# Kernel optimization log

Measured on AMD Instinct MI355X. Metric: run time of the kernel, lower is better.

The kernel has to match this reference:

```python
import jax, jax.numpy as jnp
import numpy as np

B, S, D, H, E = 4, 2048, 512, 1024, 8


def setup_inputs() -> dict:
    key = jax.random.key(0)
    ks = jax.random.split(key, 4)
    x = jax.random.normal(ks[0], (B, S, D), jnp.float32)
    Wr = jax.random.normal(ks[1], (E, D), jnp.float32) * 0.02   # router weight [E, D]
    br = jnp.zeros((E,), jnp.float32)
    W1 = jax.random.normal(ks[2], (E, D, H), jnp.float32) * 0.02  # fc1 per expert
    b1 = jnp.zeros((E, H), jnp.float32)
    W2 = jax.random.normal(ks[3], (E, H, D), jnp.float32) * 0.02  # fc2 per expert
    b2 = jnp.zeros((E, D), jnp.float32)
    return {"x": x, "Wr": Wr, "br": br, "W1": W1, "b1": b1, "W2": W2, "b2": b2}


def reference(x, Wr, br, W1, b1, W2, b2):
    # world_size == 1: every all_to_all is the identity; the pipeline reduces to
    # y[t] = sum_{k in top2} gate_k(t) * Expert_{idx_k(t)}(x[t])
    b, s, d = x.shape
    n = b * s
    e = Wr.shape[0]
    xf = x.reshape(n, d)                                   # (N, D)
    logits = xf @ Wr.T + br                                # (N, E)
    probs = jax.nn.softmax(logits, axis=-1)
    top2_prob, top2_idx = jax.lax.top_k(probs, 2)          # (N, 2) each, same tie-break as torch.topk
    # combine weights: comb[t, e] = sum_k gate_tk * [idx_tk == e]
    comb = jnp.zeros((n, e), x.dtype).at[jnp.arange(n)[:, None], top2_idx].add(top2_prob)
    # dense grouped-expert FFN (exact erf-GELU, matching torch F.gelu default)
    h = jax.nn.gelu(jnp.einsum('nd,edh->enh', xf, W1) + b1[:, None, :], approximate=False)
    o = jnp.einsum('enh,ehd->end', h, W2) + b2[:, None, :]  # (E, N, D)
    y = jnp.einsum('ne,end->nd', comb, o)                   # gate-weighted combine
    return y.reshape(b, s, d)
```

## Files before the change

### kernel.cpp

```cpp
#include <hip/hip_runtime.h>
#include <hip/hip_bf16.h>
#include <math.h>

#define N_TOK 8192
#define DIM   512
#define HID   1024
#define NEXP  8
#define CSTRIDE 32
#define NBLK  32
#define TCAP  80

typedef __attribute__((ext_vector_type(8))) __bf16 bf16x8;
typedef __attribute__((ext_vector_type(4))) float  f32x4;

static __device__ __forceinline__ unsigned short f2bf(float f) {
    unsigned int u = __builtin_bit_cast(unsigned int, f);
    unsigned int r = u + 0x7fffu + ((u >> 16) & 1u);
    return (unsigned short)(r >> 16);
}
static __device__ __forceinline__ float bf2f(unsigned short s) {
    unsigned int u = ((unsigned int)s) << 16;
    return __builtin_bit_cast(float, u);
}

__global__ __launch_bounds__(256) void prep_router_kernel(
    const float* __restrict__ x, const float* __restrict__ Wr,
    const float* __restrict__ br,
    const float* __restrict__ W1, const float* __restrict__ W2,
    unsigned short* __restrict__ xb,
    unsigned short* __restrict__ W1p, unsigned short* __restrict__ W2p,
    int* __restrict__ counts, int* __restrict__ tlist, float* __restrict__ glist)
{
    __shared__ unsigned short lt[32][128];
    __shared__ float lg[32][8];
    __shared__ int lcnt[8];
    __shared__ int lbase[8];
    int bid = blockIdx.x;
    int tin = threadIdx.x;
    if (bid < 2048) {
        int e, kb, seg, OUTD;
        const float* W;
        if (bid < 1024) {
            e = bid >> 7; kb = (bid >> 3) & 15; seg = bid & 7;
            OUTD = HID;
            W = W1 + (size_t)e * DIM * HID + (size_t)(kb * 32) * HID + seg * 128;
        } else {
            int b = bid - 1024;
            e = b >> 7; kb = (b >> 2) & 31; seg = b & 3;
            OUTD = DIM;
            W = W2 + (size_t)e * HID * DIM + (size_t)(kb * 32) * DIM + seg * 128;
        }
        #pragma unroll
        for (int i = 0; i < 4; i++) {
            int fl = i * 256 + tin;
            int r = fl >> 5, c4 = fl & 31;
            float4 v = *reinterpret_cast<const float4*>(W + (size_t)r * OUTD + c4 * 4);
            lt[r][c4*4+0] = f2bf(v.x); lt[r][c4*4+1] = f2bf(v.y);
            lt[r][c4*4+2] = f2bf(v.z); lt[r][c4*4+3] = f2bf(v.w);
        }
        __syncthreads();
        unsigned short* dstp = (bid < 1024) ? W1p : W2p;
        #pragma unroll
        for (int i = 0; i < 2; i++) {
            int s = i * 256 + tin;
            int nbl = s >> 6, l = s & 63;
            unsigned short u[8];
            #pragma unroll
            for (int j = 0; j < 8; j++) u[j] = lt[(l >> 4) * 8 + j][nbl * 16 + (l & 15)];
            size_t o;
            if (bid < 1024) o = (((size_t)((bid>>7) * 64 + (bid&7) * 8 + nbl) * 16 + ((bid>>3)&15)) * 64 + l) * 8;
            else { int b2_ = bid - 1024;
                   o = (((size_t)((b2_>>7) * 32 + (b2_&3) * 8 + nbl) * 32 + ((b2_>>2)&31)) * 64 + l) * 8; }
            *reinterpret_cast<uint4*>(dstp + o) = *reinterpret_cast<const uint4*>(u);
        }
        return;
    }
    int rb = bid - 2048;
    int slot = tin >> 3, e = tin & 7;
    int t0 = rb * 32;
    int t = t0 + slot;
    if (tin < 8) lcnt[tin] = 0;
    const float4* xr = (const float4*)(x + (size_t)t * DIM);
    const float4* wr = (const float4*)(Wr + (size_t)e * DIM);
    float acc = 0.f;
    #pragma unroll 4
    for (int i = 0; i < DIM / 4; i++) {
        float4 a = xr[i], b = wr[i];
        acc += a.x * b.x + a.y * b.y + a.z * b.z + a.w * b.w;
    }
    acc += br[e];
    lg[slot][e] = acc;
    __syncthreads();
    int i1 = 0, i2 = 0, l1 = 0, l2 = 0;
    float p1 = 0.f, p2 = 0.f;
    if (e == 0) {
        float l0[8];
        #pragma unroll
        for (int i = 0; i < 8; i++) l0[i] = lg[slot][i];
        float m1 = l0[0];
        #pragma unroll
        for (int i = 1; i < 8; i++) if (l0[i] > m1) { m1 = l0[i]; i1 = i; }
        float sum = 0.f;
        #pragma unroll
        for (int i = 0; i < 8; i++) sum += expf(l0[i] - m1);
        float m2 = -1e30f;
        #pragma unroll
        for (int i = 0; i < 8; i++) if (i != i1 && l0[i] > m2) { m2 = l0[i]; i2 = i; }
        float inv = 1.f / sum;
        p1 = inv;
        p2 = expf(m2 - m1) * inv;
        l1 = atomicAdd(&lcnt[i1], 1);
        l2 = atomicAdd(&lcnt[i2], 1);
    }
    __syncthreads();
    if (tin < 8) lbase[tin] = atomicAdd(&counts[tin * CSTRIDE], lcnt[tin]);
    __syncthreads();
    if (e == 0) {
        int pos1 = lbase[i1] + l1;
        tlist[i1 * N_TOK + pos1] = t * 2;     glist[i1 * N_TOK + pos1] = p1;
        int pos2 = lbase[i2] + l2;
        tlist[i2 * N_TOK + pos2] = t * 2 + 1; glist[i2 * N_TOK + pos2] = p2;
    }
    #pragma unroll
    for (int i = 0; i < 8; i++) {
        int flat = i * 256 + tin;
        int row = flat >> 6, c8 = flat & 63;
        const float4* src = (const float4*)(x + (size_t)(t0 + row) * DIM + c8 * 8);
        float4 a = src[0], b = src[1];
        unsigned short u[8];
        u[0]=f2bf(a.x); u[1]=f2bf(a.y); u[2]=f2bf(a.z); u[3]=f2bf(a.w);
        u[4]=f2bf(b.x); u[5]=f2bf(b.y); u[6]=f2bf(b.z); u[7]=f2bf(b.w);
        *reinterpret_cast<uint4*>(xb + (size_t)(t0 + row) * DIM + c8 * 8) =
            *reinterpret_cast<const uint4*>(u);
    }
}

__global__ __launch_bounds__(512, 2) void ffn_kernel(
    const unsigned short* __restrict__ xb,
    const unsigned short* __restrict__ W1p,
    const unsigned short* __restrict__ W2p,
    const float* __restrict__ b1, const float* __restrict__ b2,
    const int* __restrict__ counts, const int* __restrict__ tlist,
    const float* __restrict__ glist, unsigned short* __restrict__ opair)
{
    const int e = blockIdx.x;
    const int cnt = counts[e * CSTRIDE];
    const int ty = blockIdx.y;
    const int m0 = (cnt * ty) >> 5;
    const int m1 = (cnt * (ty + 1)) >> 5;
    const int nvalid = m1 - m0;
    if (nvalid <= 0) return;

    __shared__ __align__(16) unsigned short xs[TCAP * 512];
    __shared__ __align__(16) unsigned short hs[TCAP * 256];
    __shared__ int   tls[TCAP];
    __shared__ float gls[TCAP];

    const int tid = threadIdx.x;
    const int w = tid >> 6, lane = tid & 63;
    const int lg_ = lane >> 4, lm = lane & 15;

    if (tid < TCAP) {
        int idx = m0 + tid;
        int src = (idx < m1) ? idx : m0;
        tls[tid] = tlist[e * N_TOK + src];
        gls[tid] = (idx < m1) ? glist[e * N_TOK + src] : 0.f;
    }
    __syncthreads();

    #pragma unroll
    for (int i = 0; i < 10; i++) {
        int row = w * 10 + i;
        uint4 v;
        if (row < nvalid) {
            int token = tls[row] >> 1;
            v = *(reinterpret_cast<const uint4*>(xb + (size_t)token * DIM) + lane);
        } else {
            v.x = v.y = v.z = v.w = 0u;
        }
        int bo = row * 1024 + ((lane * 16) ^ ((row & 7) << 4));
        *reinterpret_cast<uint4*>(reinterpret_cast<char*>(xs) + bo) = v;
    }
    __syncthreads();

    const char* xsb = reinterpret_cast<const char*>(xs);
    char* hsb = reinterpret_cast<char*>(hs);

    f32x4 acc2[4][5];
    #pragma unroll
    for (int a = 0; a < 4; a++)
        #pragma unroll
        for (int b = 0; b < 5; b++) acc2[a][b] = (f32x4)0.f;

    for (int c = 0; c < 4; c++) {
        f32x4 acc1[2][5];
        #pragma unroll
        for (int a = 0; a < 2; a++)
            #pragma unroll
            for (int b = 0; b < 5; b++) acc1[a][b] = (f32x4)0.f;
        const uint4* w1base = reinterpret_cast<const uint4*>(W1p)
            + ((size_t)(e * 64 + c * 16 + w * 2) * 16) * 64 + lane;
        #pragma unroll
        for (int kb = 0; kb < 16; kb++) {
            bf16x8 aw[2];
            #pragma unroll
            for (int i = 0; i < 2; i++)
                aw[i] = __builtin_bit_cast(bf16x8, w1base[(size_t)(i * 16 + kb) * 64]);
            #pragma unroll
            for (int tt = 0; tt < 5; tt++) {
                int row = tt * 16 + lm;
                int bo = row * 1024 + ((kb * 64 + lg_ * 16) ^ ((row & 7) << 4));
                bf16x8 bx = __builtin_bit_cast(bf16x8,
                    *reinterpret_cast<const uint4*>(xsb + bo));
                #pragma unroll
                for (int i = 0; i < 2; i++)
                    acc1[i][tt] = __builtin_amdgcn_mfma_f32_16x16x32_bf16(aw[i], bx, acc1[i][tt], 0, 0, 0);
            }
        }
        __syncthreads();
        #pragma unroll
        for (int i = 0; i < 2; i++) {
            int hloc0 = (w * 2 + i) * 16 + lg_ * 4;
            f32x4 b1v = *reinterpret_cast<const f32x4*>(b1 + (size_t)e * HID + c * 256 + hloc0);
            #pragma unroll
            for (int tt = 0; tt < 5; tt++) {
                int trow = tt * 16 + lm;
                float g[4];
                #pragma unroll
                for (int r = 0; r < 4; r++) {
                    float v = acc1[i][tt][r] + b1v[r];
                    g[r] = 0.5f * v * (1.f + erff(v * 0.7071067811865475f));
                }
                unsigned int p0 = (unsigned int)f2bf(g[0]) | ((unsigned int)f2bf(g[1]) << 16);
                unsigned int p1 = (unsigned int)f2bf(g[2]) | ((unsigned int)f2bf(g[3]) << 16);
                unsigned long long pk = (unsigned long long)p0 | ((unsigned long long)p1 << 32);
                int bo = trow * 512 + ((hloc0 * 2) ^ ((trow & 7) << 4));
                *reinterpret_cast<unsigned long long*>(hsb + bo) = pk;
            }
        }
        __syncthreads();
        const uint4* w2base = reinterpret_cast<const uint4*>(W2p)
            + ((size_t)(e * 32 + w * 4) * 32 + c * 8) * 64 + lane;
        #pragma unroll
        for (int kb = 0; kb < 8; kb++) {
            bf16x8 aw2[4];
            #pragma unroll
            for (int j = 0; j < 4; j++)
                aw2[j] = __builtin_bit_cast(bf16x8, w2base[(size_t)(j * 32 + kb) * 64]);
            #pragma unroll
            for (int tt = 0; tt < 5; tt++) {
                int row = tt * 16 + lm;
                int bo = row * 512 + ((kb * 64 + lg_ * 16) ^ ((row & 7) << 4));
                bf16x8 bh = __builtin_bit_cast(bf16x8,
                    *reinterpret_cast<const uint4*>(hsb + bo));
                #pragma unroll
                for (int j = 0; j < 4; j++)
                    acc2[j][tt] = __builtin_amdgcn_mfma_f32_16x16x32_bf16(aw2[j], bh, acc2[j][tt], 0, 0, 0);
            }
        }
    }

    #pragma unroll
    for (int j = 0; j < 4; j++) {
        int dbase = (w * 4 + j) * 16 + lg_ * 4;
        f32x4 b2v = *reinterpret_cast<const f32x4*>(b2 + (size_t)e * DIM + dbase);
        #pragma unroll
        for (int tt = 0; tt < 5; tt++) {
            int trow = tt * 16 + lm;
            if (trow < nvalid) {
                int   ent = tls[trow];
                float gt  = gls[trow];
                float o0 = gt * (acc2[j][tt][0] + b2v[0]);
                float o1 = gt * (acc2[j][tt][1] + b2v[1]);
                float o2 = gt * (acc2[j][tt][2] + b2v[2]);
                float o3 = gt * (acc2[j][tt][3] + b2v[3]);
                uint2 pk;
                pk.x = (unsigned int)f2bf(o0) | ((unsigned int)f2bf(o1) << 16);
                pk.y = (unsigned int)f2bf(o2) | ((unsigned int)f2bf(o3) << 16);
                *reinterpret_cast<uint2*>(opair + (size_t)ent * DIM + dbase) = pk;
            }
        }
    }
}

__global__ __launch_bounds__(256) void combine_kernel(
    const unsigned short* __restrict__ opair, float* __restrict__ y)
{
    int n = blockIdx.x * 256 + threadIdx.x;
    int t = n >> 6, c8 = n & 63;
    uint4 a = *reinterpret_cast<const uint4*>(opair + (size_t)(t * 2) * DIM + c8 * 8);
    uint4 b = *reinterpret_cast<const uint4*>(opair + (size_t)(t * 2 + 1) * DIM + c8 * 8);
    float4 r0, r1;
    r0.x = bf2f((unsigned short)(a.x      )) + bf2f((unsigned short)(b.x      ));
    r0.y = bf2f((unsigned short)(a.x >> 16)) + bf2f((unsigned short)(b.x >> 16));
    r0.z = bf2f((unsigned short)(a.y      )) + bf2f((unsigned short)(b.y      ));
    r0.w = bf2f((unsigned short)(a.y >> 16)) + bf2f((unsigned short)(b.y >> 16));
    r1.x = bf2f((unsigned short)(a.z      )) + bf2f((unsigned short)(b.z      ));
    r1.y = bf2f((unsigned short)(a.z >> 16)) + bf2f((unsigned short)(b.z >> 16));
    r1.z = bf2f((unsigned short)(a.w      )) + bf2f((unsigned short)(b.w      ));
    r1.w = bf2f((unsigned short)(a.w >> 16)) + bf2f((unsigned short)(b.w >> 16));
    float4* dst = reinterpret_cast<float4*>(y + (size_t)t * DIM + c8 * 8);
    dst[0] = r0; dst[1] = r1;
}

extern "C" void kernel_launch(void* const* d_in, const int* in_sizes, int n_in,
                              void* d_out, int out_size, void* d_ws, size_t ws_size,
                              hipStream_t stream)
{
    const float* x  = (const float*)d_in[0];
    const float* Wr = (const float*)d_in[1];
    const float* br = (const float*)d_in[2];
    const float* W1 = (const float*)d_in[3];
    const float* b1 = (const float*)d_in[4];
    const float* W2 = (const float*)d_in[5];
    const float* b2 = (const float*)d_in[6];
    float* y = (float*)d_out;

    char* ws = (char*)d_ws;
    int*   counts = (int*)ws;
    int*   tlist  = (int*)(ws + 1024);
    float* glist  = (float*)(ws + 1024 + 262144);
    unsigned short* xb  = (unsigned short*)(ws + 1024 + 524288);
    unsigned short* W1p = xb  + (size_t)N_TOK * DIM;
    unsigned short* W2p = W1p + (size_t)NEXP * DIM * HID;
    unsigned short* opair = W2p + (size_t)NEXP * HID * DIM;

    hipMemsetAsync(counts, 0, NEXP * CSTRIDE * sizeof(int), stream);
    prep_router_kernel<<<2304, 256, 0, stream>>>(x, Wr, br, W1, W2, xb,
                                                 W1p, W2p, counts, tlist, glist);
    ffn_kernel<<<dim3(8, NBLK), 512, 0, stream>>>(xb, W1p, W2p, b1, b2,
                                                  counts, tlist, glist, opair);
    combine_kernel<<<2048, 256, 0, stream>>>(opair, y);
}
```

Measured before the change: 122.0 us.

## Fuse x bf16 conversion into FFN gather and restructure router block layout

Drops the separate bf16 copy of x. The FFN kernel now gathers fp32 token rows and converts them to bf16 while loading into shared memory. The router now runs first, on 256 blocks, with 8 lanes per token splitting the D dimension and reducing by shuffle, and weight-packing blocks are reordered so the expert index varies fastest. The FFN also skips MFMA work for 16-row tiles beyond the valid token count and drops the 2-block occupancy hint. This saves a write and re-read of x in bf16, but the FFN gather now reads twice the bytes per token.

```diff
diff --git a/kernel.cpp b/kernel.cpp
--- a/kernel.cpp
+++ b/kernel.cpp
@@ -27,116 +27,113 @@
     const float* __restrict__ x, const float* __restrict__ Wr,
     const float* __restrict__ br,
     const float* __restrict__ W1, const float* __restrict__ W2,
-    unsigned short* __restrict__ xb,
     unsigned short* __restrict__ W1p, unsigned short* __restrict__ W2p,
     int* __restrict__ counts, int* __restrict__ tlist, float* __restrict__ glist)
 {
     __shared__ unsigned short lt[32][128];
-    __shared__ float lg[32][8];
     __shared__ int lcnt[8];
     __shared__ int lbase[8];
     int bid = blockIdx.x;
     int tin = threadIdx.x;
-    if (bid < 2048) {
-        int e, kb, seg, OUTD;
-        const float* W;
-        if (bid < 1024) {
-            e = bid >> 7; kb = (bid >> 3) & 15; seg = bid & 7;
-            OUTD = HID;
-            W = W1 + (size_t)e * DIM * HID + (size_t)(kb * 32) * HID + seg * 128;
-        } else {
-            int b = bid - 1024;
-            e = b >> 7; kb = (b >> 2) & 31; seg = b & 3;
-            OUTD = DIM;
-            W = W2 + (size_t)e * HID * DIM + (size_t)(kb * 32) * DIM + seg * 128;
-        }
-        #pragma unroll
-        for (int i = 0; i < 4; i++) {
-            int fl = i * 256 + tin;
-            int r = fl >> 5, c4 = fl & 31;
-            float4 v = *reinterpret_cast<const float4*>(W + (size_t)r * OUTD + c4 * 4);
-            lt[r][c4*4+0] = f2bf(v.x); lt[r][c4*4+1] = f2bf(v.y);
-            lt[r][c4*4+2] = f2bf(v.z); lt[r][c4*4+3] = f2bf(v.w);
-        }
-        __syncthreads();
-        unsigned short* dstp = (bid < 1024) ? W1p : W2p;
-        #pragma unroll
-        for (int i = 0; i < 2; i++) {
-            int s = i * 256 + tin;
-            int nbl = s >> 6, l = s & 63;
-            unsigned short u[8];
-            #pragma unroll
-            for (int j = 0; j < 8; j++) u[j] = lt[(l >> 4) * 8 + j][nbl * 16 + (l & 15)];
-            size_t o;
-            if (bid < 1024) o = (((size_t)((bid>>7) * 64 + (bid&7) * 8 + nbl) * 16 + ((bid>>3)&15)) * 64 + l) * 8;
-            else { int b2_ = bid - 1024;
-                   o = (((size_t)((b2_>>7) * 32 + (b2_&3) * 8 + nbl) * 32 + ((b2_>>2)&31)) * 64 + l) * 8; }
-            *reinterpret_cast<uint4*>(dstp + o) = *reinterpret_cast<const uint4*>(u);
+    if (bid < 256) {
+        int slot = tin >> 3, es = tin & 7;
+        int t = bid * 32 + slot;
+        if (tin < 8) lcnt[tin] = 0;
+        const float4* xr = (const float4*)(x + (size_t)t * DIM + es * 64);
+        float4 xv[16];
+        #pragma unroll
+        for (int i = 0; i < 16; i++) xv[i] = xr[i];
+        float part[8];
+        #pragma unroll
+        for (int ed = 0; ed < 8; ed++) {
+            const float4* wrp = (const float4*)(Wr + (size_t)ed * DIM + es * 64);
+            float a = 0.f;
+            #pragma unroll
+            for (int i = 0; i < 16; i++) {
+                float4 b = wrp[i];
+                a += xv[i].x*b.x + xv[i].y*b.y + xv[i].z*b.z + xv[i].w*b.w;
+            }
+            part[ed] = a;
+        }
+        #pragma unroll
+        for (int m = 1; m < 8; m <<= 1) {
+            #pragma unroll
+            for (int ed = 0; ed < 8; ed++)
+                part[ed] += __shfl_xor(part[ed], m, 64);
+        }
+        int i1 = 0, i2 = 0, l1 = 0, l2 = 0;
+        float p1 = 0.f, p2 = 0.f;
+        __syncthreads();
+        if (es == 0) {
+            float l0[8];
+            #pragma unroll
+            for (int i = 0; i < 8; i++) l0[i] = part[i] + br[i];
+            float m1v = l0[0];
+            #pragma unroll
+            for (int i = 1; i < 8; i++) if (l0[i] > m1v) { m1v = l0[i]; i1 = i; }
+            float sum = 0.f;
+            #pragma unroll
+            for (int i = 0; i < 8; i++) sum += expf(l0[i] - m1v);
+            float m2v = -1e30f;
+            #pragma unroll
+            for (int i = 0; i < 8; i++) if (i != i1 && l0[i] > m2v) { m2v = l0[i]; i2 = i; }
+            float inv = 1.f / sum;
+            p1 = inv;
+            p2 = expf(m2v - m1v) * inv;
+            l1 = atomicAdd(&lcnt[i1], 1);
+            l2 = atomicAdd(&lcnt[i2], 1);
+        }
+        __syncthreads();
+        if (tin < 8) lbase[tin] = atomicAdd(&counts[tin * CSTRIDE], lcnt[tin]);
+        __syncthreads();
+        if (es == 0) {
+            int pos1 = lbase[i1] + l1;
+            tlist[i1 * N_TOK + pos1] = t * 2;     glist[i1 * N_TOK + pos1] = p1;
+            int pos2 = lbase[i2] + l2;
+            tlist[i2 * N_TOK + pos2] = t * 2 + 1; glist[i2 * N_TOK + pos2] = p2;
         }
         return;
     }
-    int rb = bid - 2048;
-    int slot = tin >> 3, e = tin & 7;
-    int t0 = rb * 32;
-    int t = t0 + slot;
-    if (tin < 8) lcnt[tin] = 0;
-    const float4* xr = (const float4*)(x + (size_t)t * DIM);
-    const float4* wr = (const float4*)(Wr + (size_t)e * DIM);
-    float acc = 0.f;
-    #pragma unroll 4
-    for (int i = 0; i < DIM / 4; i++) {
-        float4 a = xr[i], b = wr[i];
-        acc += a.x * b.x + a.y * b.y + a.z * b.z + a.w * b.w;
-    }
-    acc += br[e];
-    lg[slot][e] = acc;
+    int e, kb, seg, OUTD;
+    const float* W;
+    bool isW1 = bid < 1280;
+    if (isW1) {
+        int b = bid - 256;
+        e = b & 7; kb = (b >> 3) & 15; seg = b >> 7;
+        OUTD = HID;
+        W = W1 + (size_t)e * DIM * HID + (size_t)(kb * 32) * HID + seg * 128;
+    } else {
+        int b = bid - 1280;
+        e = b & 7; kb = (b >> 3) & 31; seg = b >> 8;
+        OUTD = DIM;
+        W = W2 + (size_t)e * HID * DIM + (size_t)(kb * 32) * DIM + seg * 128;
+    }
+    #pragma unroll
+    for (int i = 0; i < 4; i++) {
+        int fl = i * 256 + tin;
+        int r = fl >> 5, c4 = fl & 31;
+        float4 v = *reinterpret_cast<const float4*>(W + (size_t)r * OUTD + c4 * 4);
+        lt[r][c4*4+0] = f2bf(v.x); lt[r][c4*4+1] = f2bf(v.y);
+        lt[r][c4*4+2] = f2bf(v.z); lt[r][c4*4+3] = f2bf(v.w);
+    }
     __syncthreads();
-    int i1 = 0, i2 = 0, l1 = 0, l2 = 0;
-    float p1 = 0.f, p2 = 0.f;
-    if (e == 0) {
-        float l0[8];
-        #pragma unroll
-        for (int i = 0; i < 8; i++) l0[i] = lg[slot][i];
-        float m1 = l0[0];
-        #pragma unroll
-        for (int i = 1; i < 8; i++) if (l0[i] > m1) { m1 = l0[i]; i1 = i; }
-        float sum = 0.f;
-        #pragma unroll
-        for (int i = 0; i < 8; i++) sum += expf(l0[i] - m1);
-        float m2 = -1e30f;
-        #pragma unroll
-        for (int i = 0; i < 8; i++) if (i != i1 && l0[i] > m2) { m2 = l0[i]; i2 = i; }
-        float inv = 1.f / sum;
-        p1 = inv;
-        p2 = expf(m2 - m1) * inv;
-        l1 = atomicAdd(&lcnt[i1], 1);
-        l2 = atomicAdd(&lcnt[i2], 1);
-    }
-    __syncthreads();
-    if (tin < 8) lbase[tin] = atomicAdd(&counts[tin * CSTRIDE], lcnt[tin]);
-    __syncthreads();
-    if (e == 0) {
-        int pos1 = lbase[i1] + l1;
-        tlist[i1 * N_TOK + pos1] = t * 2;     glist[i1 * N_TOK + pos1] = p1;
-        int pos2 = lbase[i2] + l2;
-        tlist[i2 * N_TOK + pos2] = t * 2 + 1; glist[i2 * N_TOK + pos2] = p2;
-    }
-    #pragma unroll
-    for (int i = 0; i < 8; i++) {
-        int flat = i * 256 + tin;
-        int row = flat >> 6, c8 = flat & 63;
-        const float4* src = (const float4*)(x + (size_t)(t0 + row) * DIM + c8 * 8);
-        float4 a = src[0], b = src[1];
+    unsigned short* dstp = isW1 ? W1p : W2p;
+    #pragma unroll
+    for (int i = 0; i < 2; i++) {
+        int s = i * 256 + tin;
+        int nbl = s >> 6, l = s & 63;
         unsigned short u[8];
-        u[0]=f2bf(a.x); u[1]=f2bf(a.y); u[2]=f2bf(a.z); u[3]=f2bf(a.w);
-        u[4]=f2bf(b.x); u[5]=f2bf(b.y); u[6]=f2bf(b.z); u[7]=f2bf(b.w);
-        *reinterpret_cast<uint4*>(xb + (size_t)(t0 + row) * DIM + c8 * 8) =
-            *reinterpret_cast<const uint4*>(u);
-    }
-}
-
-__global__ __launch_bounds__(512, 2) void ffn_kernel(
-    const unsigned short* __restrict__ xb,
+        #pragma unroll
+        for (int j = 0; j < 8; j++) u[j] = lt[(l >> 4) * 8 + j][nbl * 16 + (l & 15)];
+        size_t o;
+        if (isW1) o = (((size_t)(e * 64 + seg * 8 + nbl) * 16 + kb) * 64 + l) * 8;
+        else      o = (((size_t)(e * 32 + seg * 8 + nbl) * 32 + kb) * 64 + l) * 8;
+        *reinterpret_cast<uint4*>(dstp + o) = *reinterpret_cast<const uint4*>(u);
+    }
+}
+
+__global__ __launch_bounds__(512) void ffn_kernel(
+    const float* __restrict__ x,
     const unsigned short* __restrict__ W1p,
     const unsigned short* __restrict__ W2p,
     const float* __restrict__ b1, const float* __restrict__ b2,
@@ -150,6 +147,7 @@
     const int m1 = (cnt * (ty + 1)) >> 5;
     const int nvalid = m1 - m0;
     if (nvalid <= 0) return;
+    const int ntiles = (nvalid + 15) >> 4;
 
     __shared__ __align__(16) unsigned short xs[TCAP * 512];
     __shared__ __align__(16) unsigned short hs[TCAP * 256];
@@ -174,7 +172,12 @@
         uint4 v;
         if (row < nvalid) {
             int token = tls[row] >> 1;
-            v = *(reinterpret_cast<const uint4*>(xb + (size_t)token * DIM) + lane);
+            const float4* xr = (const float4*)(x + (size_t)token * DIM) + lane * 2;
+            float4 a = xr[0], b = xr[1];
+            unsigned short u[8];
+            u[0]=f2bf(a.x); u[1]=f2bf(a.y); u[2]=f2bf(a.z); u[3]=f2bf(a.w);
+            u[4]=f2bf(b.x); u[5]=f2bf(b.y); u[6]=f2bf(b.z); u[7]=f2bf(b.w);
+            v = *reinterpret_cast<const uint4*>(u);
         } else {
             v.x = v.y = v.z = v.w = 0u;
         }
@@ -208,13 +211,15 @@
                 aw[i] = __builtin_bit_cast(bf16x8, w1base[(size_t)(i * 16 + kb) * 64]);
             #pragma unroll
             for (int tt = 0; tt < 5; tt++) {
-                int row = tt * 16 + lm;
-                int bo = row * 1024 + ((kb * 64 + lg_ * 16) ^ ((row & 7) << 4));
-                bf16x8 bx = __builtin_bit_cast(bf16x8,
-                    *reinterpret_cast<const uint4*>(xsb + bo));
-                #pragma unroll
-                for (int i = 0; i < 2; i++)
-                    acc1[i][tt] = __builtin_amdgcn_mfma_f32_16x16x32_bf16(aw[i], bx, acc1[i][tt], 0, 0, 0);
+                if (tt < ntiles) {
+                    int row = tt * 16 + lm;
+                    int bo = row * 1024 + ((kb * 64 + lg_ * 16) ^ ((row & 7) << 4));
+                    bf16x8 bx = __builtin_bit_cast(bf16x8,
+                        *reinterpret_cast<const uint4*>(xsb + bo));
+                    #pragma unroll
+                    for (int i = 0; i < 2; i++)
+                        acc1[i][tt] = __builtin_amdgcn_mfma_f32_16x16x32_bf16(aw[i], bx, acc1[i][tt], 0, 0, 0);
+                }
             }
         }
         __syncthreads();
@@ -224,18 +229,20 @@
             f32x4 b1v = *reinterpret_cast<const f32x4*>(b1 + (size_t)e * HID + c * 256 + hloc0);
             #pragma unroll
             for (int tt = 0; tt < 5; tt++) {
-                int trow = tt * 16 + lm;
-                float g[4];
-                #pragma unroll
-                for (int r = 0; r < 4; r++) {
-                    float v = acc1[i][tt][r] + b1v[r];
-                    g[r] = 0.5f * v * (1.f + erff(v * 0.7071067811865475f));
+                if (tt < ntiles) {
+                    int trow = tt * 16 + lm;
+                    float g[4];
+                    #pragma unroll
+                    for (int r = 0; r < 4; r++) {
+                        float v = acc1[i][tt][r] + b1v[r];
+                        g[r] = 0.5f * v * (1.f + erff(v * 0.7071067811865475f));
+                    }
+                    unsigned int p0 = (unsigned int)f2bf(g[0]) | ((unsigned int)f2bf(g[1]) << 16);
+                    unsigned int p1 = (unsigned int)f2bf(g[2]) | ((unsigned int)f2bf(g[3]) << 16);
+                    unsigned long long pk = (unsigned long long)p0 | ((unsigned long long)p1 << 32);
+                    int bo = trow * 512 + ((hloc0 * 2) ^ ((trow & 7) << 4));
+                    *reinterpret_cast<unsigned long long*>(hsb + bo) = pk;
                 }
-                unsigned int p0 = (unsigned int)f2bf(g[0]) | ((unsigned int)f2bf(g[1]) << 16);
-                unsigned int p1 = (unsigned int)f2bf(g[2]) | ((unsigned int)f2bf(g[3]) << 16);
-                unsigned long long pk = (unsigned long long)p0 | ((unsigned long long)p1 << 32);
-                int bo = trow * 512 + ((hloc0 * 2) ^ ((trow & 7) << 4));
-                *reinterpret_cast<unsigned long long*>(hsb + bo) = pk;
             }
         }
         __syncthreads();
@@ -249,13 +256,15 @@
                 aw2[j] = __builtin_bit_cast(bf16x8, w2base[(size_t)(j * 32 + kb) * 64]);
             #pragma unroll
             for (int tt = 0; tt < 5; tt++) {
-                int row = tt * 16 + lm;
-                int bo = row * 512 + ((kb * 64 + lg_ * 16) ^ ((row & 7) << 4));
-                bf16x8 bh = __builtin_bit_cast(bf16x8,
-                    *reinterpret_cast<const uint4*>(hsb + bo));
-                #pragma unroll
-                for (int j = 0; j < 4; j++)
-                    acc2[j][tt] = __builtin_amdgcn_mfma_f32_16x16x32_bf16(aw2[j], bh, acc2[j][tt], 0, 0, 0);
+                if (tt < ntiles) {
+                    int row = tt * 16 + lm;
+                    int bo = row * 512 + ((kb * 64 + lg_ * 16) ^ ((row & 7) << 4));
+                    bf16x8 bh = __builtin_bit_cast(bf16x8,
+                        *reinterpret_cast<const uint4*>(hsb + bo));
+                    #pragma unroll
+                    for (int j = 0; j < 4; j++)
+                        acc2[j][tt] = __builtin_amdgcn_mfma_f32_16x16x32_bf16(aw2[j], bh, acc2[j][tt], 0, 0, 0);
+                }
             }
         }
     }
@@ -320,15 +329,14 @@
     int*   counts = (int*)ws;
     int*   tlist  = (int*)(ws + 1024);
     float* glist  = (float*)(ws + 1024 + 262144);
-    unsigned short* xb  = (unsigned short*)(ws + 1024 + 524288);
-    unsigned short* W1p = xb  + (size_t)N_TOK * DIM;
+    unsigned short* W1p = (unsigned short*)(ws + 1024 + 524288);
     unsigned short* W2p = W1p + (size_t)NEXP * DIM * HID;
     unsigned short* opair = W2p + (size_t)NEXP * HID * DIM;
 
     hipMemsetAsync(counts, 0, NEXP * CSTRIDE * sizeof(int), stream);
-    prep_router_kernel<<<2304, 256, 0, stream>>>(x, Wr, br, W1, W2, xb,
+    prep_router_kernel<<<2304, 256, 0, stream>>>(x, Wr, br, W1, W2,
                                                  W1p, W2p, counts, tlist, glist);
-    ffn_kernel<<<dim3(8, NBLK), 512, 0, stream>>>(xb, W1p, W2p, b1, b2,
+    ffn_kernel<<<dim3(8, NBLK), 512, 0, stream>>>(x, W1p, W2p, b1, b2,
                                                   counts, tlist, glist, opair);
     combine_kernel<<<2048, 256, 0, stream>>>(opair, y);
 }
```

New measurement: 129.2 us. 1.06x slower.
